# Performance work log

Measured on AMD Instinct MI355X. Metric: run time of the kernel, lower is better.

Reference implementation:

```python
import jax, jax.numpy as jnp
import numpy as np

B, L, D, H = 2, 2048, 2048, 16
DH = D // H  # 128


def setup_inputs() -> dict:
    key = jax.random.key(0)
    k1, k2 = jax.random.split(key)
    inputs = jax.random.normal(k1, (B, L, D), dtype=jnp.float32)
    # additive causal mask: 0 on/below diagonal, -inf above (matches typical usage)
    neg = jnp.finfo(jnp.float32).min
    causal = jnp.where(jnp.tril(jnp.ones((L, L), dtype=bool)), 0.0, neg)
    attn_mask = causal[None, None, :, :].astype(jnp.float32)
    # torch Linear(d, 3d, bias=False): y = x @ W.T; here W_qkv is stored as [d, 3d]
    W_qkv = jax.random.normal(k2, (D, 3 * D), dtype=jnp.float32) * (1.0 / np.sqrt(D))
    return {"inputs": inputs, "attn_mask": attn_mask, "W_qkv": W_qkv}


def reference(inputs, attn_mask, W_qkv):
    b, l, d = inputs.shape
    qkv = inputs @ W_qkv                       # [B, L, 3D]
    qkv = qkv.reshape(b, l, H, 3 * DH)         # [B, L, H, 3*dh]
    qkv = qkv.transpose(0, 2, 1, 3)            # [B, H, L, 3*dh]
    Q, K, V = jnp.split(qkv, 3, axis=-1)       # each [B, H, L, dh]
    scale = jnp.sqrt(jnp.float32(DH))
    scores = jnp.einsum("bhqd,bhkd->bhqk", Q, K) / scale
    scores = scores + attn_mask
    probs = jax.nn.softmax(scores, axis=-1)    # dropout is identity in eval / p=0
    out = jnp.einsum("bhqk,bhkd->bhqd", probs, V)
    out = out.transpose(0, 2, 1, 3).reshape(b, l, d)
    return out
```

## Files before the change

### kernel.cpp

```cpp
#include <hip/hip_runtime.h>

#define SEQL 2048
#define NHEAD 16
#define N3 6144
#define KDIM 2048

typedef __attribute__((ext_vector_type(8))) short bf16x8;
typedef __attribute__((ext_vector_type(4))) float f32x4;
typedef __attribute__((ext_vector_type(16))) float f32x16;
typedef __attribute__((ext_vector_type(4))) unsigned short us4;
typedef __attribute__((ext_vector_type(4))) float fl4;
typedef __attribute__((ext_vector_type(4))) unsigned int u32x4;

__device__ __forceinline__ unsigned short f2bf(float x) {
    unsigned u = __builtin_bit_cast(unsigned, x);
    u += 0x7fffu + ((u >> 16) & 1u);
    return (unsigned short)(u >> 16);
}

__device__ __forceinline__ void gload16(const void* g, void* l) {
    __builtin_amdgcn_global_load_lds(
        (const __attribute__((address_space(1))) unsigned int*)g,
        (__attribute__((address_space(3))) unsigned int*)l,
        16, 0, 0);
}

__device__ __forceinline__ unsigned cvtpk_bf16(float lo, float hi) {
    unsigned r;
    asm("v_cvt_pk_bf16_f32 %0, %1, %2" : "=v"(r) : "v"(lo), "v"(hi));
    return r;
}
__device__ __forceinline__ void plane32_swap(unsigned &a, unsigned &b) {
    asm("v_permlane32_swap_b32 %0, %1" : "+v"(a), "+v"(b));
}

__global__ __launch_bounds__(256) void k_convert_x(const float* __restrict__ in,
                                                   unsigned short* __restrict__ out) {
    int tid = blockIdx.x * 256 + threadIdx.x;
    const fl4* in4 = (const fl4*)in;
    us4* out4 = (us4*)out;
#pragma unroll
    for (int j = 0; j < 4; ++j) {
        int idx = tid + j * 524288;
        fl4 v = in4[idx];
        us4 o;
        o.x = f2bf(v.x); o.y = f2bf(v.y); o.z = f2bf(v.z); o.w = f2bf(v.w);
        out4[idx] = o;
    }
}

__global__ __launch_bounds__(256) void k_transpose_w(const float* __restrict__ W,
                                                     unsigned short* __restrict__ Wt) {
    __shared__ alignas(16) unsigned short Ts[64 * 68];
    int t = threadIdx.x;
    int n0 = blockIdx.x * 64;
    int k0 = blockIdx.y * 64;
    int r = t >> 2, c4 = t & 3;
#pragma unroll
    for (int j = 0; j < 4; ++j) {
        int c = (c4 + j * 4) * 4;
        fl4 v = *(const fl4*)&W[(size_t)(k0 + r) * N3 + n0 + c];
        Ts[r * 68 + c + 0] = f2bf(v.x);
        Ts[r * 68 + c + 1] = f2bf(v.y);
        Ts[r * 68 + c + 2] = f2bf(v.z);
        Ts[r * 68 + c + 3] = f2bf(v.w);
    }
    __syncthreads();
#pragma unroll
    for (int j = 0; j < 2; ++j) {
        int chunk = c4 + j * 4;
#pragma unroll
        for (int h = 0; h < 2; ++h) {
            us4 o;
            o.x = Ts[(chunk * 8 + h * 4 + 0) * 68 + r];
            o.y = Ts[(chunk * 8 + h * 4 + 1) * 68 + r];
            o.z = Ts[(chunk * 8 + h * 4 + 2) * 68 + r];
            o.w = Ts[(chunk * 8 + h * 4 + 3) * 68 + r];
            *(us4*)&Wt[(size_t)(n0 + r) * KDIM + k0 + chunk * 8 + h * 4] = o;
        }
    }
}

__global__ __launch_bounds__(256) void k_gemm_qkv(const unsigned short* __restrict__ Xb,
                                                  const unsigned short* __restrict__ Wt,
                                                  unsigned short* __restrict__ Qb,
                                                  unsigned short* __restrict__ Kb,
                                                  unsigned short* __restrict__ Vt) {
    __shared__ alignas(16) unsigned short smem[16384];
    unsigned short* As = smem;
    unsigned short* Bs = smem + 8192;
    int t = threadIdx.x;
    int wid = t >> 6, lane = t & 63, g = lane >> 4, l15 = lane & 15;
    int bid = blockIdx.x;
    bid = (bid & 7) * 192 + (bid >> 3);
    int tm = (bid & 31) * 128;
    int tn = (bid >> 5) * 128;
    const unsigned short* Ab = Xb + (size_t)tm * KDIM;
    const unsigned short* Bb = Wt + (size_t)tn * KDIM;
    int wr = wid >> 1, wc = wid & 1;
    f32x4 acc[4][4];
#pragma unroll
    for (int i = 0; i < 4; ++i)
#pragma unroll
        for (int j = 0; j < 4; ++j) acc[i][j] = (f32x4){0.f, 0.f, 0.f, 0.f};

    for (int k0 = 0; k0 < KDIM; k0 += 64) {
#pragma unroll
        for (int j = 0; j < 4; ++j) {
            int p = j * 4096 + t * 16;
            int row = p >> 7;
            int sl = ((p >> 4) & 7) ^ (row & 7);
            gload16(Ab + (size_t)row * KDIM + k0 + sl * 8,
                    (char*)As + j * 4096 + wid * 1024);
            gload16(Bb + (size_t)row * KDIM + k0 + sl * 8,
                    (char*)Bs + j * 4096 + wid * 1024);
        }
        __syncthreads();
#pragma unroll
        for (int ks = 0; ks < 2; ++ks) {
            bf16x8 af[4], bfr[4];
#pragma unroll
            for (int i = 0; i < 4; ++i) {
                int ra = wr * 64 + i * 16 + l15;
                af[i] = *(const bf16x8*)((const char*)As + ra * 128 +
                                         (((ks * 4 + g) ^ (ra & 7)) << 4));
                int rb = wc * 64 + i * 16 + l15;
                bfr[i] = *(const bf16x8*)((const char*)Bs + rb * 128 +
                                          (((ks * 4 + g) ^ (rb & 7)) << 4));
            }
#pragma unroll
            for (int i = 0; i < 4; ++i)
#pragma unroll
                for (int j = 0; j < 4; ++j)
                    acc[i][j] = __builtin_amdgcn_mfma_f32_16x16x32_bf16(
                        af[i], bfr[j], acc[i][j], 0, 0, 0);
        }
        __syncthreads();
    }
    int ty = (tn >> 7) % 3;
    int h  = tn / 384;
    int b  = tm >> 11, lp0 = tm & 2047;
    const float qsc = 0.08838834764831845f * 1.44269504089f;
#pragma unroll
    for (int i = 0; i < 4; ++i)
#pragma unroll
        for (int j = 0; j < 4; ++j) {
            int d = wc * 64 + j * 16 + l15;
#pragma unroll
            for (int r = 0; r < 4; ++r) {
                int mm = wr * 64 + i * 16 + g * 4 + r;
                float v = acc[i][j][r];
                unsigned short bv = f2bf(ty == 0 ? v * qsc : v);
                int byte;
                if (ty == 2)
                    byte = d * 256 + ((((mm >> 3) ^ (d & 15)) & 15) << 4) + (mm & 7) * 2;
                else
                    byte = mm * 256 + ((((d >> 3) ^ (mm & 15)) & 15) << 4) + (d & 7) * 2;
                *(unsigned short*)((char*)smem + byte) = bv;
            }
        }
    __syncthreads();
    int rr = t >> 1;
#pragma unroll
    for (int c = 0; c < 8; ++c) {
        int cc = (t & 1) * 8 + c;
        bf16x8 vv = *(const bf16x8*)((char*)smem + rr * 256 +
                                     (((cc ^ (rr & 15)) & 15) << 4));
        if (ty == 2) {
            int kt = (lp0 >> 6) + (cc >> 3);
            *(bf16x8*)&Vt[((size_t)((b * NHEAD + h) * 32 + kt) * 128 + rr) * 64 +
                          (cc & 7) * 8] = vv;
        } else {
            unsigned short* dst = (ty == 0) ? Qb : Kb;
            *(bf16x8*)&dst[((size_t)(b * NHEAD + h) * SEQL + lp0 + rr) * 128 + cc * 8] = vv;
        }
    }
}

__global__ __launch_bounds__(256) void k_attn(const unsigned short* __restrict__ Qb,
                                              const unsigned short* __restrict__ Kb,
                                              const unsigned short* __restrict__ Vt,
                                              float* __restrict__ out) {
    __shared__ alignas(16) unsigned short Ks[64 * 128];
    __shared__ alignas(16) unsigned short Vs[128 * 64];
    __shared__ float Fx[4][32];
    int t = threadIdx.x, w = t >> 6, lane = t & 63;
    int l31 = lane & 31, hi = lane >> 5;
    int qi = 15 - (int)blockIdx.x;
    int bh = blockIdx.y;
    int qb = qi * 128;
    int qg = qb + w * 32 + l31;
    int qwmin = qb + w * 32, qwmax = qwmin + 31;

    bf16x8 qf[8];
    const unsigned short* Qp = Qb + (size_t)(bh * SEQL + qg) * 128;
#pragma unroll
    for (int ks = 0; ks < 8; ++ks)
        qf[ks] = *(const bf16x8*)(Qp + ks * 16 + hi * 8);

    f32x16 accO[4];
#pragma unroll
    for (int db = 0; db < 4; ++db)
#pragma unroll
        for (int e = 0; e < 16; ++e) accO[db][e] = 0.f;
    float mstate = -3.0e38f, lsum = 0.f;

    int nkv = 2 * qi + 2;
    for (int kt = 0; kt < nkv; ++kt) {
        int kv0 = kt * 64;
#pragma unroll
        for (int j = 0; j < 4; ++j) {
            int p = j * 4096 + t * 16;
            int rk = p >> 8;
            int sk = ((p >> 4) & 15) ^ (rk & 15);
            gload16(Kb + (size_t)(bh * SEQL + kv0 + rk) * 128 + sk * 8,
                    (char*)Ks + j * 4096 + w * 1024);
            int rv = p >> 7;
            int sv = ((p >> 4) & 7) ^ (rv & 7);
            gload16(Vt + ((size_t)(bh * 32 + (kv0 >> 6)) * 128 + rv) * 64 + sv * 8,
                    (char*)Vs + j * 4096 + w * 1024);
        }
        __syncthreads();

        if (kv0 <= qwmax) {
            f32x16 s[2];
#pragma unroll
            for (int blk = 0; blk < 2; ++blk)
#pragma unroll
                for (int e = 0; e < 16; ++e) s[blk][e] = 0.f;
#pragma unroll
            for (int ks = 0; ks < 8; ++ks) {
                int c = ks * 2 + hi;
#pragma unroll
                for (int blk = 0; blk < 2; ++blk) {
                    int row = blk * 32 + l31;
                    bf16x8 kf = *(const bf16x8*)((const char*)Ks + row * 256 +
                                                 (((c ^ (row & 15)) & 15) << 4));
                    s[blk] = __builtin_amdgcn_mfma_f32_32x32x16_bf16(kf, qf[ks], s[blk], 0, 0, 0);
                }
            }
            if (kv0 + 63 > qwmin) {
#pragma unroll
                for (int blk = 0; blk < 2; ++blk)
#pragma unroll
                    for (int r = 0; r < 16; ++r) {
                        int kvg = kv0 + blk * 32 + (r & 3) + 8 * (r >> 2) + 4 * hi;
                        if (kvg > qg) s[blk][r] = -3.0e38f;
                    }
            }
            float tmax = -3.0e38f;
#pragma unroll
            for (int blk = 0; blk < 2; ++blk)
#pragma unroll
                for (int r = 0; r < 16; ++r) tmax = fmaxf(tmax, s[blk][r]);
            tmax = fmaxf(tmax, __shfl_xor(tmax, 32));
            if (__any(tmax > mstate + 8.0f)) {
                float mnew = fmaxf(mstate, tmax);
                float fs = __builtin_amdgcn_exp2f(mstate - mnew);
                lsum *= fs;
                mstate = mnew;
                Fx[w][l31] = fs;
                f32x4 fv[4];
#pragma unroll
                for (int q4 = 0; q4 < 4; ++q4)
                    fv[q4] = *(const f32x4*)&Fx[w][q4 * 8 + 4 * hi];
#pragma unroll
                for (int db = 0; db < 4; ++db)
#pragma unroll
                    for (int r = 0; r < 16; ++r)
                        accO[db][r] *= fv[r >> 2][r & 3];
            }
            float ps = 0.f;
#pragma unroll
            for (int blk = 0; blk < 2; ++blk)
#pragma unroll
                for (int r = 0; r < 16; ++r) {
                    float p = __builtin_amdgcn_exp2f(s[blk][r] - mstate);
                    s[blk][r] = p;
                    ps += p;
                }
            ps += __shfl_xor(ps, 32);
            lsum += ps;
            unsigned pa[4][4];
#pragma unroll
            for (int blk = 0; blk < 2; ++blk)
#pragma unroll
                for (int hf = 0; hf < 2; ++hf) {
                    int o = hf * 8;
                    unsigned d0 = cvtpk_bf16(s[blk][o + 0], s[blk][o + 1]);
                    unsigned d2 = cvtpk_bf16(s[blk][o + 4], s[blk][o + 5]);
                    plane32_swap(d0, d2);
                    unsigned d1 = cvtpk_bf16(s[blk][o + 2], s[blk][o + 3]);
                    unsigned d3 = cvtpk_bf16(s[blk][o + 6], s[blk][o + 7]);
                    plane32_swap(d1, d3);
                    pa[blk * 2 + hf][0] = d0; pa[blk * 2 + hf][1] = d1;
                    pa[blk * 2 + hf][2] = d2; pa[blk * 2 + hf][3] = d3;
                }
#pragma unroll
            for (int ksv = 0; ksv < 4; ++ksv) {
                u32x4 pu = {pa[ksv][0], pa[ksv][1], pa[ksv][2], pa[ksv][3]};
                bf16x8 paf = __builtin_bit_cast(bf16x8, pu);
                int c = ksv * 2 + hi;
#pragma unroll
                for (int db = 0; db < 4; ++db) {
                    int rv = db * 32 + l31;
                    bf16x8 vf = *(const bf16x8*)((const char*)Vs + rv * 128 +
                                                 (((c ^ (rv & 7)) & 7) << 4));
                    accO[db] = __builtin_amdgcn_mfma_f32_32x32x16_bf16(paf, vf, accO[db], 0, 0, 0);
                }
            }
        }
        __syncthreads();
    }
    float inv = 1.0f / lsum;
    Fx[w][l31] = inv;
    f32x4 iv[4];
#pragma unroll
    for (int q4 = 0; q4 < 4; ++q4)
        iv[q4] = *(const f32x4*)&Fx[w][q4 * 8 + 4 * hi];
    int b = bh >> 4, h = bh & 15;
    float* ob = out + (size_t)(b * SEQL + qb + w * 32) * 2048 + h * 128;
#pragma unroll
    for (int db = 0; db < 4; ++db)
#pragma unroll
        for (int r = 0; r < 16; ++r) {
            int qr = (r & 3) + 8 * (r >> 2) + 4 * hi;
            ob[(size_t)qr * 2048 + db * 32 + l31] = accO[db][r] * iv[r >> 2][r & 3];
        }
}

extern "C" void kernel_launch(void* const* d_in, const int* in_sizes, int n_in,
                              void* d_out, int out_size, void* d_ws, size_t ws_size,
                              hipStream_t stream) {
    const float* x = (const float*)d_in[0];
    const float* w = (const float*)d_in[2];
    float* out = (float*)d_out;
    char* ws = (char*)d_ws;
    unsigned short* Xb = (unsigned short*)(ws);
    unsigned short* Wt = (unsigned short*)(ws + 16777216);
    unsigned short* Qb = (unsigned short*)(ws + 41943040);
    unsigned short* Kb = (unsigned short*)(ws + 58720256);
    unsigned short* Vt = (unsigned short*)(ws + 75497472);

    hipLaunchKernelGGL(k_convert_x, dim3(2048), dim3(256), 0, stream, x, Xb);
    hipLaunchKernelGGL(k_transpose_w, dim3(96, 32), dim3(256), 0, stream, w, Wt);
    hipLaunchKernelGGL(k_gemm_qkv, dim3(1536), dim3(256), 0, stream, Xb, Wt, Qb, Kb, Vt);
    hipLaunchKernelGGL(k_attn, dim3(16, 32), dim3(256), 0, stream, Qb, Kb, Vt, out);
}
```

Before: 375.8 us.

## Double-buffer QKV GEMM with 256x128 tiles and 512-thread blocks

The QKV projection GEMM now uses 256x128 output tiles computed by 8 waves, where it previously used 128x128 tiles with 4 waves. It double-buffers the LDS staging of A/B tiles so the next K-tile's async global->LDS loads overlap the current tile's MFMAs, with explicit vmcnt waits and raw barriers. MFMA issue gets raised s_setprio. The epilogue is reworked for the larger tile, and 96KB of LDS limits occupancy to two blocks per CU.

Measured after the change: 362.4 us. -3.6%, faster.

```diff
diff --git a/kernel.cpp b/kernel.cpp
--- a/kernel.cpp
+++ b/kernel.cpp
@@ -81,22 +81,20 @@
     }
 }
 
-__global__ __launch_bounds__(256) void k_gemm_qkv(const unsigned short* __restrict__ Xb,
-                                                  const unsigned short* __restrict__ Wt,
-                                                  unsigned short* __restrict__ Qb,
-                                                  unsigned short* __restrict__ Kb,
-                                                  unsigned short* __restrict__ Vt) {
-    __shared__ alignas(16) unsigned short smem[16384];
-    unsigned short* As = smem;
-    unsigned short* Bs = smem + 8192;
+__global__ __launch_bounds__(512, 2) void k_gemm_qkv(const unsigned short* __restrict__ Xb,
+                                                     const unsigned short* __restrict__ Wt,
+                                                     unsigned short* __restrict__ Qb,
+                                                     unsigned short* __restrict__ Kb,
+                                                     unsigned short* __restrict__ Vt) {
+    __shared__ alignas(16) char smem[98304];
     int t = threadIdx.x;
     int wid = t >> 6, lane = t & 63, g = lane >> 4, l15 = lane & 15;
     int bid = blockIdx.x;
-    bid = (bid & 7) * 192 + (bid >> 3);
-    int tm = (bid & 31) * 128;
-    int tn = (bid >> 5) * 128;
-    const unsigned short* Ab = Xb + (size_t)tm * KDIM;
-    const unsigned short* Bb = Wt + (size_t)tn * KDIM;
+    bid = (bid & 7) * 96 + (bid >> 3);
+    int tmi = bid & 15, tni = bid >> 4;
+    int tm = tmi * 256, tn = tni * 128;
+    const unsigned short* Abase = Xb + (size_t)tm * KDIM;
+    const unsigned short* Bbase = Wt + (size_t)tn * KDIM;
     int wr = wid >> 1, wc = wid & 1;
     f32x4 acc[4][4];
 #pragma unroll
@@ -104,41 +102,65 @@
 #pragma unroll
         for (int j = 0; j < 4; ++j) acc[i][j] = (f32x4){0.f, 0.f, 0.f, 0.f};
 
-    for (int k0 = 0; k0 < KDIM; k0 += 64) {
+    auto STAGE = [&](int tile, int d) {
+        int k0 = tile * 64;
+        char* A = smem + d * 49152;
+        char* B = A + 32768;
 #pragma unroll
         for (int j = 0; j < 4; ++j) {
-            int p = j * 4096 + t * 16;
+            int p = j * 8192 + t * 16;
             int row = p >> 7;
             int sl = ((p >> 4) & 7) ^ (row & 7);
-            gload16(Ab + (size_t)row * KDIM + k0 + sl * 8,
-                    (char*)As + j * 4096 + wid * 1024);
-            gload16(Bb + (size_t)row * KDIM + k0 + sl * 8,
-                    (char*)Bs + j * 4096 + wid * 1024);
-        }
-        __syncthreads();
+            gload16(Abase + (size_t)row * KDIM + k0 + sl * 8, A + j * 8192 + wid * 1024);
+        }
+#pragma unroll
+        for (int j = 0; j < 2; ++j) {
+            int p = j * 8192 + t * 16;
+            int row = p >> 7;
+            int sl = ((p >> 4) & 7) ^ (row & 7);
+            gload16(Bbase + (size_t)row * KDIM + k0 + sl * 8, B + j * 8192 + wid * 1024);
+        }
+    };
+
+    STAGE(0, 0);
+    for (int tt = 0; tt < 32; ++tt) {
+        int cur = tt & 1;
+        if (tt < 31) {
+            STAGE(tt + 1, cur ^ 1);
+            asm volatile("s_waitcnt vmcnt(6)" ::: "memory");
+        } else {
+            asm volatile("s_waitcnt vmcnt(0)" ::: "memory");
+        }
+        __builtin_amdgcn_s_barrier();
+        asm volatile("" ::: "memory");
+        const char* A = smem + cur * 49152;
+        const char* B = A + 32768;
 #pragma unroll
         for (int ks = 0; ks < 2; ++ks) {
             bf16x8 af[4], bfr[4];
 #pragma unroll
             for (int i = 0; i < 4; ++i) {
                 int ra = wr * 64 + i * 16 + l15;
-                af[i] = *(const bf16x8*)((const char*)As + ra * 128 +
-                                         (((ks * 4 + g) ^ (ra & 7)) << 4));
+                af[i] = *(const bf16x8*)(A + ra * 128 + (((ks * 4 + g) ^ (ra & 7)) << 4));
                 int rb = wc * 64 + i * 16 + l15;
-                bfr[i] = *(const bf16x8*)((const char*)Bs + rb * 128 +
-                                          (((ks * 4 + g) ^ (rb & 7)) << 4));
-            }
+                bfr[i] = *(const bf16x8*)(B + rb * 128 + (((ks * 4 + g) ^ (rb & 7)) << 4));
+            }
+            __builtin_amdgcn_s_setprio(1);
 #pragma unroll
             for (int i = 0; i < 4; ++i)
 #pragma unroll
                 for (int j = 0; j < 4; ++j)
                     acc[i][j] = __builtin_amdgcn_mfma_f32_16x16x32_bf16(
                         af[i], bfr[j], acc[i][j], 0, 0, 0);
-        }
-        __syncthreads();
-    }
-    int ty = (tn >> 7) % 3;
-    int h  = tn / 384;
+            __builtin_amdgcn_s_setprio(0);
+        }
+        asm volatile("" ::: "memory");
+        __builtin_amdgcn_s_barrier();
+        asm volatile("" ::: "memory");
+    }
+
+    int ty = tni % 3;
+    int h  = tni / 3;
     int b  = tm >> 11, lp0 = tm & 2047;
     const float qsc = 0.08838834764831845f * 1.44269504089f;
 #pragma unroll
@@ -153,26 +175,31 @@
                 unsigned short bv = f2bf(ty == 0 ? v * qsc : v);
                 int byte;
                 if (ty == 2)
-                    byte = d * 256 + ((((mm >> 3) ^ (d & 15)) & 15) << 4) + (mm & 7) * 2;
+                    byte = d * 512 + ((((mm >> 3) ^ (d & 31)) & 31) << 4) + (mm & 7) * 2;
                 else
                     byte = mm * 256 + ((((d >> 3) ^ (mm & 15)) & 15) << 4) + (d & 7) * 2;
-                *(unsigned short*)((char*)smem + byte) = bv;
+                *(unsigned short*)(smem + byte) = bv;
             }
         }
     __syncthreads();
-    int rr = t >> 1;
-#pragma unroll
-    for (int c = 0; c < 8; ++c) {
-        int cc = (t & 1) * 8 + c;
-        bf16x8 vv = *(const bf16x8*)((char*)smem + rr * 256 +
-                                     (((cc ^ (rr & 15)) & 15) << 4));
-        if (ty == 2) {
-            int kt = (lp0 >> 6) + (cc >> 3);
-            *(bf16x8*)&Vt[((size_t)((b * NHEAD + h) * 32 + kt) * 128 + rr) * 64 +
-                          (cc & 7) * 8] = vv;
-        } else {
-            unsigned short* dst = (ty == 0) ? Qb : Kb;
-            *(bf16x8*)&dst[((size_t)(b * NHEAD + h) * SEQL + lp0 + rr) * 128 + cc * 8] = vv;
+    if (ty == 2) {
+#pragma unroll
+        for (int c = 0; c < 8; ++c) {
+            int id = c * 512 + t;
+            int d = id >> 5, L = id & 31;
+            bf16x8 vv = *(const bf16x8*)(smem + d * 512 + (((L ^ (d & 31)) & 31) << 4));
+            int kt = (lp0 >> 6) + (L >> 3);
+            *(bf16x8*)&Vt[(size_t)((b * NHEAD + h) * 32 + kt) * 8192 + d * 64 +
+                          (L & 7) * 8] = vv;
+        }
+    } else {
+        unsigned short* dst = (ty == 0) ? Qb : Kb;
+#pragma unroll
+        for (int c = 0; c < 8; ++c) {
+            int id = c * 512 + t;
+            int mm = id >> 4, cc = id & 15;
+            bf16x8 vv = *(const bf16x8*)(smem + mm * 256 + (((cc ^ (mm & 15)) & 15) << 4));
+            *(bf16x8*)&dst[((size_t)(b * NHEAD + h) * SEQL + lp0 + mm) * 128 + cc * 8] = vv;
         }
     }
 }
@@ -344,6 +371,6 @@
 
     hipLaunchKernelGGL(k_convert_x, dim3(2048), dim3(256), 0, stream, x, Xb);
     hipLaunchKernelGGL(k_transpose_w, dim3(96, 32), dim3(256), 0, stream, w, Wt);
-    hipLaunchKernelGGL(k_gemm_qkv, dim3(1536), dim3(256), 0, stream, Xb, Wt, Qb, Kb, Vt);
+    hipLaunchKernelGGL(k_gemm_qkv, dim3(768), dim3(512), 0, stream, Xb, Wt, Qb, Kb, Vt);
     hipLaunchKernelGGL(k_attn, dim3(16, 32), dim3(256), 0, stream, Qb, Kb, Vt, out);
 }
```
